# Optimization experiments

Measured on AMD Instinct MI355X. Metric: run time of the kernel, lower is better.

## Reference

```python
import jax, jax.numpy as jnp
import numpy as np
from jax import lax

N = 50000       # nodes
E = 1600000     # edges
D_IN = 1024     # input feature size
H = 256         # hidden size
L = 64          # GCN2Conv layers
C = 4           # n_classes
ALPHA = 0.2
THETA = 0.5


def setup_inputs() -> dict:
    key = jax.random.key(0)
    ks = jax.random.split(key, 7)
    x = jax.random.normal(ks[0], (N, D_IN), dtype=jnp.float32)
    edge_index = jax.random.randint(ks[1], (2, E), 0, N, dtype=jnp.int32)
    proj_W = jax.random.normal(ks[2], (D_IN, H), dtype=jnp.float32) * 0.02
    proj_b = jnp.zeros((H,), dtype=jnp.float32)
    weights = jax.random.normal(ks[3], (L, H, H), dtype=jnp.float32) * 0.05
    cls_W = jax.random.normal(ks[4], (H, C), dtype=jnp.float32) * 0.05
    cls_b = jnp.zeros((C,), dtype=jnp.float32)
    return {"x": x, "edge_index": edge_index, "proj_W": proj_W,
            "proj_b": proj_b, "weights": weights, "cls_W": cls_W, "cls_b": cls_b}


def reference(x, edge_index, proj_W, proj_b, weights, cls_W, cls_b):
    # Dropout is identity in eval mode (reference baseline).
    src, dst = edge_index[0], edge_index[1]
    # gcn_norm with added self-loops: A_hat = D^{-1/2} (A + I) D^{-1/2}
    loops = jnp.arange(N, dtype=src.dtype)
    src_f = jnp.concatenate([src, loops])
    dst_f = jnp.concatenate([dst, loops])
    deg = jax.ops.segment_sum(jnp.ones((E + N,), jnp.float32), dst_f, num_segments=N)
    dinv = jnp.where(deg > 0, lax.rsqrt(deg), 0.0)
    norm = dinv[src_f] * dinv[dst_f]  # [E+N]

    h0 = x @ proj_W + proj_b          # project: [N, H]
    betas = jnp.log(THETA / jnp.arange(1, L + 1, dtype=jnp.float32) + 1.0)  # [L]

    def step(h, wb):
        W, beta = wb
        # propagate: out[i] = sum_{(j->i)} norm * h[j]
        agg = jax.ops.segment_sum(norm[:, None] * h[src_f], dst_f, num_segments=N)
        s = (1.0 - ALPHA) * agg + ALPHA * h0     # initial residual
        h = (1.0 - beta) * s + beta * (s @ W)    # identity mapping (shared weights)
        return jax.nn.relu(h), None

    h, _ = lax.scan(step, h0, (weights, betas))
    out = h @ cls_W + cls_b  # classifier: [N, C]
    return out
```

## Files before the change

kernel.cpp:

```cpp
#include <hip/hip_runtime.h>
#include <math.h>

#define N_NODES 50000
#define N_EDGES 1600000
#define DIN 1024
#define H 256
#define L_LAYERS 64
#define ALPHA 0.2f
#define NCHUNK 8
#define CCOLS 32

typedef unsigned short u16;
typedef short short8 __attribute__((ext_vector_type(8)));
typedef unsigned short ushort8_t __attribute__((ext_vector_type(8)));
typedef float f32x4 __attribute__((ext_vector_type(4)));
typedef float f32x2 __attribute__((ext_vector_type(2)));
typedef unsigned int u32x4 __attribute__((ext_vector_type(4)));

__device__ inline float b2f(u16 h) { return __uint_as_float(((unsigned)h) << 16); }
__device__ inline u16 f2b(float f) {
  unsigned u = __float_as_uint(f);
  unsigned r = u + 0x7FFFu + ((u >> 16) & 1u);
  return (u16)(r >> 16);
}

__device__ inline f32x2 bp2f(unsigned u) {
  f32x2 p;
  p[0] = __uint_as_float(u << 16);
  p[1] = __uint_as_float(u & 0xFFFF0000u);
  return p;
}

__device__ inline size_t bidx(int node, int col) {
  return ((size_t)(col >> 5) * N_NODES + node) * CCOLS + (col & 31);
}

__global__ void GCNIIForDialog_18923625906417_kernel() {}

__global__ __launch_bounds__(256) void k_zero(int* __restrict__ p, int n) {
  int i = blockIdx.x * 256 + threadIdx.x;
  if (i < n) p[i] = 0;
}

__global__ __launch_bounds__(256) void k_count(const int* __restrict__ dst, int* __restrict__ cnt) {
  int e = blockIdx.x * 256 + threadIdx.x;
  if (e < N_EDGES) atomicAdd(&cnt[dst[e]], 1);
}

__global__ __launch_bounds__(256) void k_dinv(const int* __restrict__ cnt, float* __restrict__ dinv) {
  int i = blockIdx.x * 256 + threadIdx.x;
  if (i < N_NODES) dinv[i] = 1.0f / sqrtf((float)(cnt[i] + 1));
}

__global__ __launch_bounds__(1024) void k_scan(const int* __restrict__ cnt, int* __restrict__ offs) {
  const int CH = (N_NODES + 1023) / 1024;
  __shared__ int sums[1024];
  int t = threadIdx.x;
  int lo = t * CH, hi = lo + CH;
  if (hi > N_NODES) hi = N_NODES;
  int s = 0;
  for (int i = lo; i < hi; ++i) s += cnt[i];
  sums[t] = s;
  __syncthreads();
  for (int d = 1; d < 1024; d <<= 1) {
    int v = (t >= d) ? sums[t - d] : 0;
    __syncthreads();
    sums[t] += v;
    __syncthreads();
  }
  int run = (t == 0) ? 0 : sums[t - 1];
  for (int i = lo; i < hi; ++i) { offs[i] = run; run += cnt[i]; }
  if (t == 0) offs[N_NODES] = sums[1023];
}

__global__ __launch_bounds__(256) void k_scatter(const int* __restrict__ src, const int* __restrict__ dst,
    const int* __restrict__ offs, int* __restrict__ cursor, const float* __restrict__ dinv,
    unsigned* __restrict__ ew) {
  int e = blockIdx.x * 256 + threadIdx.x;
  if (e >= N_EDGES) return;
  int sN = src[e], dN = dst[e];
  int pos = offs[dN] + atomicAdd(&cursor[dN], 1);
  unsigned wb = (unsigned)f2b(dinv[sN] * dinv[dN]);
  ew[pos] = (wb << 16) | (unsigned)sN;
}

__global__ void k_wtr(const float* __restrict__ Win, u16* __restrict__ Wout) {
  __shared__ float tile[32][33];
  size_t base = (size_t)blockIdx.z * H * H;
  int n0 = blockIdx.x * 32, k0 = blockIdx.y * 32;
  for (int i = threadIdx.y; i < 32; i += 8)
    tile[i][threadIdx.x] = Win[base + (size_t)(k0 + i) * H + n0 + threadIdx.x];
  __syncthreads();
  for (int i = threadIdx.y; i < 32; i += 8)
    Wout[base + (size_t)(n0 + i) * H + k0 + threadIdx.x] = f2b(tile[threadIdx.x][i]);
}

__global__ void k_trP(const float* __restrict__ Win, u16* __restrict__ Wout) {
  __shared__ float tile[32][33];
  int n0 = blockIdx.x * 32, k0 = blockIdx.y * 32;
  for (int i = threadIdx.y; i < 32; i += 8)
    tile[i][threadIdx.x] = Win[(size_t)(k0 + i) * H + n0 + threadIdx.x];
  __syncthreads();
  for (int i = threadIdx.y; i < 32; i += 8)
    Wout[(size_t)(n0 + i) * DIN + k0 + threadIdx.x] = f2b(tile[threadIdx.x][i]);
}

__global__ __launch_bounds__(256) void k_spmm(
    const u16* __restrict__ hb, const u16* __restrict__ h0b,
    const int* __restrict__ offs, const unsigned* __restrict__ ew,
    const float* __restrict__ dinv, u16* __restrict__ sbb)
{
  int bid = blockIdx.x;
  int chunk = bid & 7;
  int nb = bid >> 3;
  int wid = threadIdx.x >> 6, lane = threadIdx.x & 63;
  int sub = lane & 3;
  int eslot = (lane >> 2) & 3;
  int nsub = lane >> 4;
  int node = nb * 16 + wid * 4 + nsub;
  if (node >= N_NODES) return;
  const u16* hc = hb + (size_t)chunk * N_NODES * CCOLS;
  const u16* hp = hc + sub * 8;
  f32x2 acc2[4] = {};
  int end = offs[node + 1];
  int i = offs[node] + eslot;
  for (; i + 12 < end; i += 16) {
    unsigned e0 = ew[i];
    unsigned e1 = ew[i + 4];
    unsigned e2 = ew[i + 8];
    unsigned e3 = ew[i + 12];
    u32x4 v0 = *(const u32x4*)(hp + (size_t)(e0 & 0xFFFFu) * CCOLS);
    u32x4 v1 = *(const u32x4*)(hp + (size_t)(e1 & 0xFFFFu) * CCOLS);
    u32x4 v2 = *(const u32x4*)(hp + (size_t)(e2 & 0xFFFFu) * CCOLS);
    u32x4 v3 = *(const u32x4*)(hp + (size_t)(e3 & 0xFFFFu) * CCOLS);
    float w0 = __uint_as_float(e0 & 0xFFFF0000u);
    float w1 = __uint_as_float(e1 & 0xFFFF0000u);
    float w2 = __uint_as_float(e2 & 0xFFFF0000u);
    float w3 = __uint_as_float(e3 & 0xFFFF0000u);
    f32x2 w0v = {w0, w0}, w1v = {w1, w1}, w2v = {w2, w2}, w3v = {w3, w3};
#pragma unroll
    for (int j = 0; j < 4; ++j) acc2[j] += w0v * bp2f(v0[j]);
#pragma unroll
    for (int j = 0; j < 4; ++j) acc2[j] += w1v * bp2f(v1[j]);
#pragma unroll
    for (int j = 0; j < 4; ++j) acc2[j] += w2v * bp2f(v2[j]);
#pragma unroll
    for (int j = 0; j < 4; ++j) acc2[j] += w3v * bp2f(v3[j]);
  }
  for (; i < end; i += 4) {
    unsigned e0 = ew[i];
    u32x4 v0 = *(const u32x4*)(hp + (size_t)(e0 & 0xFFFFu) * CCOLS);
    float w0 = __uint_as_float(e0 & 0xFFFF0000u);
    f32x2 w0v = {w0, w0};
#pragma unroll
    for (int j = 0; j < 4; ++j) acc2[j] += w0v * bp2f(v0[j]);
  }
#pragma unroll
  for (int d = 4; d <= 8; d <<= 1)
#pragma unroll
    for (int j = 0; j < 4; ++j) {
      acc2[j][0] += __shfl_xor(acc2[j][0], d);
      acc2[j][1] += __shfl_xor(acc2[j][1], d);
    }
  if (eslot == 0) {
    float di = dinv[node];
    float di2 = di * di;
    size_t ci = (size_t)chunk * N_NODES * CCOLS + (size_t)node * CCOLS + sub * 8;
    ushort8_t hv = *(const ushort8_t*)(hp + (size_t)node * CCOLS);
    ushort8_t h0v = __builtin_nontemporal_load((const ushort8_t*)(h0b + ci));
    ushort8_t o;
#pragma unroll
    for (int j = 0; j < 4; ++j) {
#pragma unroll
      for (int c = 0; c < 2; ++c) {
        int k = 2 * j + c;
        float v = (1.0f - ALPHA) * (acc2[j][c] + di2 * b2f(hv[k])) + ALPHA * b2f(h0v[k]);
        o[k] = f2b(v);
      }
    }
    __builtin_nontemporal_store(o, (ushort8_t*)(sbb + ci));
  }
}

__global__ __launch_bounds__(256) void k_gemm(
    const u16* __restrict__ A, const u16* __restrict__ BT,
    u16* __restrict__ Hout, float beta)
{
  __shared__ u16 As[128 * 40];
  __shared__ u16 Bs[128 * 40];
  int tid = threadIdx.x;
  int mBase = blockIdx.x * 128, nBase = blockIdx.y * 128;
  int wid = tid >> 6, lane = tid & 63;
  int wm = (wid & 1) * 64, wn = (wid >> 1) * 64;
  int lrow = lane & 15, quad = lane >> 4;
  f32x4 acc[4][4] = {};
  int sr = tid >> 2, sc = tid & 3;
  for (int k0 = 0; k0 < H; k0 += 32) {
    const u16* Ac = A + (size_t)(k0 >> 5) * N_NODES * CCOLS;
#pragma unroll
    for (int it = 0; it < 2; ++it) {
      int r = sr + it * 64;
      int grow = mBase + r;
      u32x4 va = {};
      if (grow < N_NODES) va = *(const u32x4*)(Ac + (size_t)grow * CCOLS + sc * 8);
      *(u32x4*)&As[r * 40 + sc * 8] = va;
      u32x4 vb = *(const u32x4*)(BT + (size_t)(nBase + r) * H + k0 + sc * 8);
      *(u32x4*)&Bs[r * 40 + sc * 8] = vb;
    }
    __syncthreads();
    short8 af[4], bfr[4];
#pragma unroll
    for (int i = 0; i < 4; ++i) {
      af[i]  = *(const short8*)&As[(wm + i * 16 + lrow) * 40 + quad * 8];
      bfr[i] = *(const short8*)&Bs[(wn + i * 16 + lrow) * 40 + quad * 8];
    }
#pragma unroll
    for (int mi = 0; mi < 4; ++mi)
#pragma unroll
      for (int ni = 0; ni < 4; ++ni)
        acc[mi][ni] = __builtin_amdgcn_mfma_f32_16x16x32_bf16(af[mi], bfr[ni], acc[mi][ni], 0, 0, 0);
    __syncthreads();
  }
#pragma unroll
  for (int mi = 0; mi < 4; ++mi)
#pragma unroll
    for (int ni = 0; ni < 4; ++ni)
#pragma unroll
      for (int rg = 0; rg < 4; ++rg) {
        int r = mBase + wm + mi * 16 + quad * 4 + rg;
        int c = nBase + wn + ni * 16 + lrow;
        if (r < N_NODES) {
          size_t idx = bidx(r, c);
          float v = (1.0f - beta) * b2f(A[idx]) + beta * acc[mi][ni][rg];
          Hout[idx] = f2b(fmaxf(v, 0.0f));
        }
      }
}

__global__ __launch_bounds__(256) void k_pgemm(
    const float* __restrict__ X, const u16* __restrict__ BT,
    const float* __restrict__ bias, u16* __restrict__ h0b, u16* __restrict__ h)
{
  __shared__ u16 As[128 * 40];
  __shared__ u16 Bs[128 * 40];
  int tid = threadIdx.x;
  int mBase = blockIdx.x * 128, nBase = blockIdx.y * 128;
  int wid = tid >> 6, lane = tid & 63;
  int wm = (wid & 1) * 64, wn = (wid >> 1) * 64;
  int lrow = lane & 15, quad = lane >> 4;
  f32x4 acc[4][4] = {};
  int sr = tid >> 2, sc = tid & 3;
  for (int k0 = 0; k0 < DIN; k0 += 32) {
#pragma unroll
    for (int it = 0; it < 2; ++it) {
      int r = sr + it * 64;
      int grow = mBase + r;
      float4 fa0 = make_float4(0.f, 0.f, 0.f, 0.f);
      float4 fa1 = make_float4(0.f, 0.f, 0.f, 0.f);
      if (grow < N_NODES) {
        const float* ap = X + (size_t)grow * DIN + k0 + sc * 8;
        fa0 = *(const float4*)ap;
        fa1 = *(const float4*)(ap + 4);
      }
      ushort8_t av;
      av[0] = f2b(fa0.x); av[1] = f2b(fa0.y); av[2] = f2b(fa0.z); av[3] = f2b(fa0.w);
      av[4] = f2b(fa1.x); av[5] = f2b(fa1.y); av[6] = f2b(fa1.z); av[7] = f2b(fa1.w);
      *(ushort8_t*)&As[r * 40 + sc * 8] = av;
      u32x4 vb = *(const u32x4*)(BT + (size_t)(nBase + r) * DIN + k0 + sc * 8);
      *(u32x4*)&Bs[r * 40 + sc * 8] = vb;
    }
    __syncthreads();
    short8 af[4], bfr[4];
#pragma unroll
    for (int i = 0; i < 4; ++i) {
      af[i]  = *(const short8*)&As[(wm + i * 16 + lrow) * 40 + quad * 8];
      bfr[i] = *(const short8*)&Bs[(wn + i * 16 + lrow) * 40 + quad * 8];
    }
#pragma unroll
    for (int mi = 0; mi < 4; ++mi)
#pragma unroll
      for (int ni = 0; ni < 4; ++ni)
        acc[mi][ni] = __builtin_amdgcn_mfma_f32_16x16x32_bf16(af[mi], bfr[ni], acc[mi][ni], 0, 0, 0);
    __syncthreads();
  }
#pragma unroll
  for (int mi = 0; mi < 4; ++mi)
#pragma unroll
    for (int ni = 0; ni < 4; ++ni)
#pragma unroll
      for (int rg = 0; rg < 4; ++rg) {
        int r = mBase + wm + mi * 16 + quad * 4 + rg;
        int c = nBase + wn + ni * 16 + lrow;
        if (r < N_NODES) {
          size_t idx = bidx(r, c);
          float v = acc[mi][ni][rg] + bias[c];
          u16 bv = f2b(v);
          h0b[idx] = bv;
          h[idx] = bv;
        }
      }
}

__global__ __launch_bounds__(256) void k_cls(const u16* __restrict__ h,
    const float* __restrict__ W, const float* __restrict__ b, float* __restrict__ out)
{
  int wid = threadIdx.x >> 6, lane = threadIdx.x & 63;
  int node = blockIdx.x * 4 + wid;
  if (node >= N_NODES) return;
  float a0 = 0, a1 = 0, a2 = 0, a3 = 0;
  for (int t = lane; t < H; t += 64) {
    float hv = b2f(h[bidx(node, t)]);
    a0 += hv * W[t * 4 + 0];
    a1 += hv * W[t * 4 + 1];
    a2 += hv * W[t * 4 + 2];
    a3 += hv * W[t * 4 + 3];
  }
#pragma unroll
  for (int off = 32; off > 0; off >>= 1) {
    a0 += __shfl_down(a0, off);
    a1 += __shfl_down(a1, off);
    a2 += __shfl_down(a2, off);
    a3 += __shfl_down(a3, off);
  }
  if (lane == 0) {
    float4 o;
    o.x = a0 + b[0];
    o.y = a1 + b[1];
    o.z = a2 + b[2];
    o.w = a3 + b[3];
    *(float4*)(out + (size_t)node * 4) = o;
  }
}

extern "C" void kernel_launch(void* const* d_in, const int* in_sizes, int n_in,
                              void* d_out, int out_size, void* d_ws, size_t ws_size,
                              hipStream_t stream) {
  (void)in_sizes; (void)n_in; (void)out_size; (void)ws_size;
  const float* x     = (const float*)d_in[0];
  const int*   ei    = (const int*)d_in[1];
  const float* projW = (const float*)d_in[2];
  const float* projB = (const float*)d_in[3];
  const float* wts   = (const float*)d_in[4];
  const float* clsW  = (const float*)d_in[5];
  const float* clsB  = (const float*)d_in[6];
  float* out = (float*)d_out;

  char* ws = (char*)d_ws;
  size_t off = 0;
  auto alloc = [&](size_t bytes) -> void* {
    void* p = ws + off;
    off = (off + bytes + 255) & ~(size_t)255;
    return p;
  };
  int*   cntcur = (int*)alloc((size_t)N_NODES * 2 * 4);
  int*   cnt    = cntcur;
  int*   cursor = cntcur + N_NODES;
  int*   offs   = (int*)alloc((size_t)(N_NODES + 1) * 4);
  float* dinv   = (float*)alloc((size_t)N_NODES * 4);
  unsigned* ew  = (unsigned*)alloc((size_t)N_EDGES * 4);
  u16*   WT     = (u16*)alloc((size_t)L_LAYERS * H * H * 2);
  u16*   BTp    = (u16*)alloc((size_t)H * DIN * 2);
  u16*   h0b    = (u16*)alloc((size_t)N_NODES * H * 2);
  u16*   sb     = (u16*)alloc((size_t)N_NODES * H * 2);
  u16*   h      = (u16*)alloc((size_t)N_NODES * H * 2);

  const int* src = ei;
  const int* dst = ei + N_EDGES;

  k_zero<<<(N_NODES * 2 + 255) / 256, 256, 0, stream>>>(cntcur, N_NODES * 2);
  k_count<<<(N_EDGES + 255) / 256, 256, 0, stream>>>(dst, cnt);
  k_dinv<<<(N_NODES + 255) / 256, 256, 0, stream>>>(cnt, dinv);
  k_scan<<<1, 1024, 0, stream>>>(cnt, offs);
  k_scatter<<<(N_EDGES + 255) / 256, 256, 0, stream>>>(src, dst, offs, cursor, dinv, ew);
  k_wtr<<<dim3(H / 32, H / 32, L_LAYERS), dim3(32, 8), 0, stream>>>(wts, WT);
  k_trP<<<dim3(H / 32, DIN / 32), dim3(32, 8), 0, stream>>>(projW, BTp);

  k_pgemm<<<dim3((N_NODES + 127) / 128, H / 128), 256, 0, stream>>>(x, BTp, projB, h0b, h);

  dim3 ggrid((N_NODES + 127) / 128, H / 128);
  const int spmm_blocks = ((N_NODES + 15) / 16) * NCHUNK;
  for (int l = 0; l < L_LAYERS; ++l) {
    k_spmm<<<spmm_blocks, 256, 0, stream>>>(h, h0b, offs, ew, dinv, sb);
    float beta = logf(0.5f / (float)(l + 1) + 1.0f);
    k_gemm<<<ggrid, 256, 0, stream>>>(sb, WT + (size_t)l * H * H, h, beta);
  }
  k_cls<<<(N_NODES + 3) / 4, 256, 0, stream>>>(h, clsW, clsB, out);
}
```

Measured before the change: 9.419 ms.

## Pad CSR rows to multiples of four and use persistent SpMM blocks

Each node's edge list in the CSR is padded to a multiple of four, with the edge array zero-filled so padding entries carry weight zero and point at node 0. Each lane can then fetch four packed edges with one 128-bit nontemporal load and the scalar tail loop goes away. The SpMM kernel also becomes a grid-stride kernel with a fixed 2048 blocks that loop over node groups per chunk, which cuts block launch overhead. The cost is extra zero-weight gathers on node 0 and a larger edge array that needs an extra zeroing pass.

Result: slower. 11.52 ms (+22.3%).

```diff
diff --git a/kernel.cpp b/kernel.cpp
--- a/kernel.cpp
+++ b/kernel.cpp
@@ -9,6 +9,9 @@
 #define ALPHA 0.2f
 #define NCHUNK 8
 #define CCOLS 32
+#define EW_CAP (N_EDGES + 4 * N_NODES)
+#define SPMM_BLOCKS 2048
+#define BLK_PER_CHUNK (SPMM_BLOCKS / NCHUNK)
 
 typedef unsigned short u16;
 typedef short short8 __attribute__((ext_vector_type(8)));
@@ -59,7 +62,7 @@
   int lo = t * CH, hi = lo + CH;
   if (hi > N_NODES) hi = N_NODES;
   int s = 0;
-  for (int i = lo; i < hi; ++i) s += cnt[i];
+  for (int i = lo; i < hi; ++i) s += (cnt[i] + 3) & ~3;
   sums[t] = s;
   __syncthreads();
   for (int d = 1; d < 1024; d <<= 1) {
@@ -69,7 +72,7 @@
     __syncthreads();
   }
   int run = (t == 0) ? 0 : sums[t - 1];
-  for (int i = lo; i < hi; ++i) { offs[i] = run; run += cnt[i]; }
+  for (int i = lo; i < hi; ++i) { offs[i] = run; run += (cnt[i] + 3) & ~3; }
   if (t == 0) offs[N_NODES] = sums[1023];
 }
 
@@ -110,75 +113,66 @@
     const int* __restrict__ offs, const unsigned* __restrict__ ew,
     const float* __restrict__ dinv, u16* __restrict__ sbb)
 {
-  int bid = blockIdx.x;
-  int chunk = bid & 7;
-  int nb = bid >> 3;
+  const int NBLK = (N_NODES + 15) / 16;
+  int chunk = blockIdx.x & 7;
+  int bslot = blockIdx.x >> 3;
   int wid = threadIdx.x >> 6, lane = threadIdx.x & 63;
   int sub = lane & 3;
   int eslot = (lane >> 2) & 3;
   int nsub = lane >> 4;
-  int node = nb * 16 + wid * 4 + nsub;
-  if (node >= N_NODES) return;
   const u16* hc = hb + (size_t)chunk * N_NODES * CCOLS;
   const u16* hp = hc + sub * 8;
-  f32x2 acc2[4] = {};
-  int end = offs[node + 1];
-  int i = offs[node] + eslot;
-  for (; i + 12 < end; i += 16) {
-    unsigned e0 = ew[i];
-    unsigned e1 = ew[i + 4];
-    unsigned e2 = ew[i + 8];
-    unsigned e3 = ew[i + 12];
-    u32x4 v0 = *(const u32x4*)(hp + (size_t)(e0 & 0xFFFFu) * CCOLS);
-    u32x4 v1 = *(const u32x4*)(hp + (size_t)(e1 & 0xFFFFu) * CCOLS);
-    u32x4 v2 = *(const u32x4*)(hp + (size_t)(e2 & 0xFFFFu) * CCOLS);
-    u32x4 v3 = *(const u32x4*)(hp + (size_t)(e3 & 0xFFFFu) * CCOLS);
-    float w0 = __uint_as_float(e0 & 0xFFFF0000u);
-    float w1 = __uint_as_float(e1 & 0xFFFF0000u);
-    float w2 = __uint_as_float(e2 & 0xFFFF0000u);
-    float w3 = __uint_as_float(e3 & 0xFFFF0000u);
-    f32x2 w0v = {w0, w0}, w1v = {w1, w1}, w2v = {w2, w2}, w3v = {w3, w3};
-#pragma unroll
-    for (int j = 0; j < 4; ++j) acc2[j] += w0v * bp2f(v0[j]);
-#pragma unroll
-    for (int j = 0; j < 4; ++j) acc2[j] += w1v * bp2f(v1[j]);
-#pragma unroll
-    for (int j = 0; j < 4; ++j) acc2[j] += w2v * bp2f(v2[j]);
-#pragma unroll
-    for (int j = 0; j < 4; ++j) acc2[j] += w3v * bp2f(v3[j]);
-  }
-  for (; i < end; i += 4) {
-    unsigned e0 = ew[i];
-    u32x4 v0 = *(const u32x4*)(hp + (size_t)(e0 & 0xFFFFu) * CCOLS);
-    float w0 = __uint_as_float(e0 & 0xFFFF0000u);
-    f32x2 w0v = {w0, w0};
-#pragma unroll
-    for (int j = 0; j < 4; ++j) acc2[j] += w0v * bp2f(v0[j]);
-  }
-#pragma unroll
-  for (int d = 4; d <= 8; d <<= 1)
-#pragma unroll
-    for (int j = 0; j < 4; ++j) {
-      acc2[j][0] += __shfl_xor(acc2[j][0], d);
-      acc2[j][1] += __shfl_xor(acc2[j][1], d);
-    }
-  if (eslot == 0) {
-    float di = dinv[node];
-    float di2 = di * di;
-    size_t ci = (size_t)chunk * N_NODES * CCOLS + (size_t)node * CCOLS + sub * 8;
-    ushort8_t hv = *(const ushort8_t*)(hp + (size_t)node * CCOLS);
-    ushort8_t h0v = __builtin_nontemporal_load((const ushort8_t*)(h0b + ci));
-    ushort8_t o;
-#pragma unroll
-    for (int j = 0; j < 4; ++j) {
-#pragma unroll
-      for (int c = 0; c < 2; ++c) {
-        int k = 2 * j + c;
-        float v = (1.0f - ALPHA) * (acc2[j][c] + di2 * b2f(hv[k])) + ALPHA * b2f(h0v[k]);
-        o[k] = f2b(v);
-      }
-    }
-    __builtin_nontemporal_store(o, (ushort8_t*)(sbb + ci));
+
+  for (int nb = bslot; nb < NBLK; nb += BLK_PER_CHUNK) {
+    int node = nb * 16 + wid * 4 + nsub;
+    if (node >= N_NODES) continue;
+    f32x2 acc2[4] = {};
+    int i0 = offs[node], end = offs[node + 1];
+    for (int i = i0 + eslot * 4; i < end; i += 16) {
+      u32x4 er = __builtin_nontemporal_load((const u32x4*)(ew + i));
+      u32x4 v0 = *(const u32x4*)(hp + (size_t)(er[0] & 0xFFFFu) * CCOLS);
+      u32x4 v1 = *(const u32x4*)(hp + (size_t)(er[1] & 0xFFFFu) * CCOLS);
+      u32x4 v2 = *(const u32x4*)(hp + (size_t)(er[2] & 0xFFFFu) * CCOLS);
+      u32x4 v3 = *(const u32x4*)(hp + (size_t)(er[3] & 0xFFFFu) * CCOLS);
+      float w0 = __uint_as_float(er[0] & 0xFFFF0000u);
+      float w1 = __uint_as_float(er[1] & 0xFFFF0000u);
+      float w2 = __uint_as_float(er[2] & 0xFFFF0000u);
+      float w3 = __uint_as_float(er[3] & 0xFFFF0000u);
+      f32x2 w0v = {w0, w0}, w1v = {w1, w1}, w2v = {w2, w2}, w3v = {w3, w3};
+#pragma unroll
+      for (int j = 0; j < 4; ++j) acc2[j] += w0v * bp2f(v0[j]);
+#pragma unroll
+      for (int j = 0; j < 4; ++j) acc2[j] += w1v * bp2f(v1[j]);
+#pragma unroll
+      for (int j = 0; j < 4; ++j) acc2[j] += w2v * bp2f(v2[j]);
+#pragma unroll
+      for (int j = 0; j < 4; ++j) acc2[j] += w3v * bp2f(v3[j]);
+    }
+#pragma unroll
+    for (int d = 4; d <= 8; d <<= 1)
+#pragma unroll
+      for (int j = 0; j < 4; ++j) {
+        acc2[j][0] += __shfl_xor(acc2[j][0], d);
+        acc2[j][1] += __shfl_xor(acc2[j][1], d);
+      }
+    if (eslot == 0) {
+      float di = dinv[node];
+      float di2 = di * di;
+      size_t ci = (size_t)chunk * N_NODES * CCOLS + (size_t)node * CCOLS + sub * 8;
+      ushort8_t hv = *(const ushort8_t*)(hp + (size_t)node * CCOLS);
+      ushort8_t h0v = __builtin_nontemporal_load((const ushort8_t*)(h0b + ci));
+      ushort8_t o;
+#pragma unroll
+      for (int j = 0; j < 4; ++j) {
+#pragma unroll
+        for (int c = 0; c < 2; ++c) {
+          int k = 2 * j + c;
+          float v = (1.0f - ALPHA) * (acc2[j][c] + di2 * b2f(hv[k])) + ALPHA * b2f(h0v[k]);
+          o[k] = f2b(v);
+        }
+      }
+      __builtin_nontemporal_store(o, (ushort8_t*)(sbb + ci));
+    }
   }
 }
 
@@ -357,7 +351,7 @@
   int*   cursor = cntcur + N_NODES;
   int*   offs   = (int*)alloc((size_t)(N_NODES + 1) * 4);
   float* dinv   = (float*)alloc((size_t)N_NODES * 4);
-  unsigned* ew  = (unsigned*)alloc((size_t)N_EDGES * 4);
+  unsigned* ew  = (unsigned*)alloc((size_t)EW_CAP * 4);
   u16*   WT     = (u16*)alloc((size_t)L_LAYERS * H * H * 2);
   u16*   BTp    = (u16*)alloc((size_t)H * DIN * 2);
   u16*   h0b    = (u16*)alloc((size_t)N_NODES * H * 2);
@@ -368,6 +362,7 @@
   const int* dst = ei + N_EDGES;
 
   k_zero<<<(N_NODES * 2 + 255) / 256, 256, 0, stream>>>(cntcur, N_NODES * 2);
+  k_zero<<<(EW_CAP + 255) / 256, 256, 0, stream>>>((int*)ew, EW_CAP);
   k_count<<<(N_EDGES + 255) / 256, 256, 0, stream>>>(dst, cnt);
   k_dinv<<<(N_NODES + 255) / 256, 256, 0, stream>>>(cnt, dinv);
   k_scan<<<1, 1024, 0, stream>>>(cnt, offs);
@@ -378,9 +373,8 @@
   k_pgemm<<<dim3((N_NODES + 127) / 128, H / 128), 256, 0, stream>>>(x, BTp, projB, h0b, h);
 
   dim3 ggrid((N_NODES + 127) / 128, H / 128);
-  const int spmm_blocks = ((N_NODES + 15) / 16) * NCHUNK;
   for (int l = 0; l < L_LAYERS; ++l) {
-    k_spmm<<<spmm_blocks, 256, 0, stream>>>(h, h0b, offs, ew, dinv, sb);
+    k_spmm<<<SPMM_BLOCKS, 256, 0, stream>>>(h, h0b, offs, ew, dinv, sb);
     float beta = logf(0.5f / (float)(l + 1) + 1.0f);
     k_gemm<<<ggrid, 256, 0, stream>>>(sb, WT + (size_t)l * H * H, h, beta);
   }
```

## Fuse SpMM aggregation and layer GEMM into one kernel with LDS-resident tile

Applied to the files above, without the earlier changes.

Merges the per-layer sparse aggregation and dense GEMM into a single kernel: each block aggregates 128 nodes across all 256 columns into shared memory, then multiplies that tile by the full weight matrix in two column halves. This removes the intermediate s buffer round trip through global memory and one launch per layer, and uses ping-pong h buffers because the gather reads h from other nodes. In exchange, grid parallelism drops from ~25k small SpMM blocks to ~391 large blocks with ~68KB of LDS each, limiting occupancy and latency hiding for the irregular gathers.

After: 19.98 ms. 2.12x slower.

```diff
diff --git a/kernel.cpp b/kernel.cpp
--- a/kernel.cpp
+++ b/kernel.cpp
@@ -9,6 +9,7 @@
 #define ALPHA 0.2f
 #define NCHUNK 8
 #define CCOLS 32
+#define SBS_STRIDE 268
 
 typedef unsigned short u16;
 typedef short short8 __attribute__((ext_vector_type(8)));
@@ -105,136 +106,140 @@
     Wout[(size_t)(n0 + i) * DIN + k0 + threadIdx.x] = f2b(tile[threadIdx.x][i]);
 }
 
-__global__ __launch_bounds__(256) void k_spmm(
+__global__ __launch_bounds__(256) void k_fused(
     const u16* __restrict__ hb, const u16* __restrict__ h0b,
     const int* __restrict__ offs, const unsigned* __restrict__ ew,
-    const float* __restrict__ dinv, u16* __restrict__ sbb)
-{
-  int bid = blockIdx.x;
-  int chunk = bid & 7;
-  int nb = bid >> 3;
-  int wid = threadIdx.x >> 6, lane = threadIdx.x & 63;
-  int sub = lane & 3;
-  int eslot = (lane >> 2) & 3;
-  int nsub = lane >> 4;
-  int node = nb * 16 + wid * 4 + nsub;
-  if (node >= N_NODES) return;
-  const u16* hc = hb + (size_t)chunk * N_NODES * CCOLS;
-  const u16* hp = hc + sub * 8;
-  f32x2 acc2[4] = {};
-  int end = offs[node + 1];
-  int i = offs[node] + eslot;
-  for (; i + 12 < end; i += 16) {
-    unsigned e0 = ew[i];
-    unsigned e1 = ew[i + 4];
-    unsigned e2 = ew[i + 8];
-    unsigned e3 = ew[i + 12];
-    u32x4 v0 = *(const u32x4*)(hp + (size_t)(e0 & 0xFFFFu) * CCOLS);
-    u32x4 v1 = *(const u32x4*)(hp + (size_t)(e1 & 0xFFFFu) * CCOLS);
-    u32x4 v2 = *(const u32x4*)(hp + (size_t)(e2 & 0xFFFFu) * CCOLS);
-    u32x4 v3 = *(const u32x4*)(hp + (size_t)(e3 & 0xFFFFu) * CCOLS);
-    float w0 = __uint_as_float(e0 & 0xFFFF0000u);
-    float w1 = __uint_as_float(e1 & 0xFFFF0000u);
-    float w2 = __uint_as_float(e2 & 0xFFFF0000u);
-    float w3 = __uint_as_float(e3 & 0xFFFF0000u);
-    f32x2 w0v = {w0, w0}, w1v = {w1, w1}, w2v = {w2, w2}, w3v = {w3, w3};
-#pragma unroll
-    for (int j = 0; j < 4; ++j) acc2[j] += w0v * bp2f(v0[j]);
-#pragma unroll
-    for (int j = 0; j < 4; ++j) acc2[j] += w1v * bp2f(v1[j]);
-#pragma unroll
-    for (int j = 0; j < 4; ++j) acc2[j] += w2v * bp2f(v2[j]);
-#pragma unroll
-    for (int j = 0; j < 4; ++j) acc2[j] += w3v * bp2f(v3[j]);
-  }
-  for (; i < end; i += 4) {
-    unsigned e0 = ew[i];
-    u32x4 v0 = *(const u32x4*)(hp + (size_t)(e0 & 0xFFFFu) * CCOLS);
-    float w0 = __uint_as_float(e0 & 0xFFFF0000u);
-    f32x2 w0v = {w0, w0};
-#pragma unroll
-    for (int j = 0; j < 4; ++j) acc2[j] += w0v * bp2f(v0[j]);
-  }
-#pragma unroll
-  for (int d = 4; d <= 8; d <<= 1)
-#pragma unroll
-    for (int j = 0; j < 4; ++j) {
-      acc2[j][0] += __shfl_xor(acc2[j][0], d);
-      acc2[j][1] += __shfl_xor(acc2[j][1], d);
-    }
-  if (eslot == 0) {
-    float di = dinv[node];
-    float di2 = di * di;
-    size_t ci = (size_t)chunk * N_NODES * CCOLS + (size_t)node * CCOLS + sub * 8;
-    ushort8_t hv = *(const ushort8_t*)(hp + (size_t)node * CCOLS);
-    ushort8_t h0v = __builtin_nontemporal_load((const ushort8_t*)(h0b + ci));
-    ushort8_t o;
-#pragma unroll
-    for (int j = 0; j < 4; ++j) {
-#pragma unroll
-      for (int c = 0; c < 2; ++c) {
-        int k = 2 * j + c;
-        float v = (1.0f - ALPHA) * (acc2[j][c] + di2 * b2f(hv[k])) + ALPHA * b2f(h0v[k]);
-        o[k] = f2b(v);
-      }
-    }
-    __builtin_nontemporal_store(o, (ushort8_t*)(sbb + ci));
-  }
-}
-
-__global__ __launch_bounds__(256) void k_gemm(
-    const u16* __restrict__ A, const u16* __restrict__ BT,
+    const float* __restrict__ dinv, const u16* __restrict__ BT,
     u16* __restrict__ Hout, float beta)
 {
-  __shared__ u16 As[128 * 40];
+  __shared__ u16 sbs[128][SBS_STRIDE];
   __shared__ u16 Bs[128 * 40];
   int tid = threadIdx.x;
-  int mBase = blockIdx.x * 128, nBase = blockIdx.y * 128;
   int wid = tid >> 6, lane = tid & 63;
+  int mBase = blockIdx.x * 128;
+
+  {
+    int sub = lane & 3;
+    int eslot = (lane >> 2) & 3;
+    int nsub = lane >> 4;
+    for (int chunk = 0; chunk < NCHUNK; ++chunk) {
+      const u16* hc = hb + (size_t)chunk * N_NODES * CCOLS;
+      const u16* hp = hc + sub * 8;
+      for (int pass = 0; pass < 8; ++pass) {
+        int lr = wid * 32 + pass * 4 + nsub;
+        int node = mBase + lr;
+        bool valid = node < N_NODES;
+        f32x2 acc2[4] = {};
+        if (valid) {
+          int end = offs[node + 1];
+          int i = offs[node] + eslot;
+          for (; i + 12 < end; i += 16) {
+            unsigned e0 = ew[i];
+            unsigned e1 = ew[i + 4];
+            unsigned e2 = ew[i + 8];
+            unsigned e3 = ew[i + 12];
+            u32x4 v0 = *(const u32x4*)(hp + (size_t)(e0 & 0xFFFFu) * CCOLS);
+            u32x4 v1 = *(const u32x4*)(hp + (size_t)(e1 & 0xFFFFu) * CCOLS);
+            u32x4 v2 = *(const u32x4*)(hp + (size_t)(e2 & 0xFFFFu) * CCOLS);
+            u32x4 v3 = *(const u32x4*)(hp + (size_t)(e3 & 0xFFFFu) * CCOLS);
+            float w0 = __uint_as_float(e0 & 0xFFFF0000u);
+            float w1 = __uint_as_float(e1 & 0xFFFF0000u);
+            float w2 = __uint_as_float(e2 & 0xFFFF0000u);
+            float w3 = __uint_as_float(e3 & 0xFFFF0000u);
+            f32x2 w0v = {w0, w0}, w1v = {w1, w1}, w2v = {w2, w2}, w3v = {w3, w3};
+#pragma unroll
+            for (int j = 0; j < 4; ++j) acc2[j] += w0v * bp2f(v0[j]);
+#pragma unroll
+            for (int j = 0; j < 4; ++j) acc2[j] += w1v * bp2f(v1[j]);
+#pragma unroll
+            for (int j = 0; j < 4; ++j) acc2[j] += w2v * bp2f(v2[j]);
+#pragma unroll
+            for (int j = 0; j < 4; ++j) acc2[j] += w3v * bp2f(v3[j]);
+          }
+          for (; i < end; i += 4) {
+            unsigned e0 = ew[i];
+            u32x4 v0 = *(const u32x4*)(hp + (size_t)(e0 & 0xFFFFu) * CCOLS);
+            float w0 = __uint_as_float(e0 & 0xFFFF0000u);
+            f32x2 w0v = {w0, w0};
+#pragma unroll
+            for (int j = 0; j < 4; ++j) acc2[j] += w0v * bp2f(v0[j]);
+          }
+        }
+#pragma unroll
+        for (int d = 4; d <= 8; d <<= 1)
+#pragma unroll
+          for (int j = 0; j < 4; ++j) {
+            acc2[j][0] += __shfl_xor(acc2[j][0], d);
+            acc2[j][1] += __shfl_xor(acc2[j][1], d);
+          }
+        if (eslot == 0) {
+          ushort8_t o = {0, 0, 0, 0, 0, 0, 0, 0};
+          if (valid) {
+            float di = dinv[node];
+            float di2 = di * di;
+            size_t ci = (size_t)chunk * N_NODES * CCOLS + (size_t)node * CCOLS + sub * 8;
+            ushort8_t hv = *(const ushort8_t*)(hp + (size_t)node * CCOLS);
+            ushort8_t h0v = __builtin_nontemporal_load((const ushort8_t*)(h0b + ci));
+#pragma unroll
+            for (int j = 0; j < 4; ++j) {
+#pragma unroll
+              for (int c = 0; c < 2; ++c) {
+                int k = 2 * j + c;
+                float v = (1.0f - ALPHA) * (acc2[j][c] + di2 * b2f(hv[k])) + ALPHA * b2f(h0v[k]);
+                o[k] = f2b(v);
+              }
+            }
+          }
+          *(ushort8_t*)&sbs[lr][chunk * 32 + sub * 8] = o;
+        }
+      }
+    }
+  }
+  __syncthreads();
+
   int wm = (wid & 1) * 64, wn = (wid >> 1) * 64;
   int lrow = lane & 15, quad = lane >> 4;
-  f32x4 acc[4][4] = {};
   int sr = tid >> 2, sc = tid & 3;
-  for (int k0 = 0; k0 < H; k0 += 32) {
-    const u16* Ac = A + (size_t)(k0 >> 5) * N_NODES * CCOLS;
-#pragma unroll
-    for (int it = 0; it < 2; ++it) {
-      int r = sr + it * 64;
-      int grow = mBase + r;
-      u32x4 va = {};
-      if (grow < N_NODES) va = *(const u32x4*)(Ac + (size_t)grow * CCOLS + sc * 8);
-      *(u32x4*)&As[r * 40 + sc * 8] = va;
-      u32x4 vb = *(const u32x4*)(BT + (size_t)(nBase + r) * H + k0 + sc * 8);
-      *(u32x4*)&Bs[r * 40 + sc * 8] = vb;
+  for (int nh = 0; nh < 2; ++nh) {
+    int nBase = nh * 128;
+    f32x4 acc[4][4] = {};
+    for (int k0 = 0; k0 < H; k0 += 32) {
+#pragma unroll
+      for (int it = 0; it < 2; ++it) {
+        int r = sr + it * 64;
+        u32x4 vb = *(const u32x4*)(BT + (size_t)(nBase + r) * H + k0 + sc * 8);
+        *(u32x4*)&Bs[r * 40 + sc * 8] = vb;
+      }
+      __syncthreads();
+      short8 af[4], bfr[4];
+#pragma unroll
+      for (int i = 0; i < 4; ++i) {
+        af[i]  = *(const short8*)&sbs[wm + i * 16 + lrow][k0 + quad * 8];
+        bfr[i] = *(const short8*)&Bs[(wn + i * 16 + lrow) * 40 + quad * 8];
+      }
+#pragma unroll
+      for (int mi = 0; mi < 4; ++mi)
+#pragma unroll
+        for (int ni = 0; ni < 4; ++ni)
+          acc[mi][ni] = __builtin_amdgcn_mfma_f32_16x16x32_bf16(af[mi], bfr[ni], acc[mi][ni], 0, 0, 0);
+      __syncthreads();
     }
-    __syncthreads();
-    short8 af[4], bfr[4];
-#pragma unroll
-    for (int i = 0; i < 4; ++i) {
-      af[i]  = *(const short8*)&As[(wm + i * 16 + lrow) * 40 + quad * 8];
-      bfr[i] = *(const short8*)&Bs[(wn + i * 16 + lrow) * 40 + quad * 8];
-    }
 #pragma unroll
     for (int mi = 0; mi < 4; ++mi)
 #pragma unroll
       for (int ni = 0; ni < 4; ++ni)
-        acc[mi][ni] = __builtin_amdgcn_mfma_f32_16x16x32_bf16(af[mi], bfr[ni], acc[mi][ni], 0, 0, 0);
-    __syncthreads();
-  }
-#pragma unroll
-  for (int mi = 0; mi < 4; ++mi)
-#pragma unroll
-    for (int ni = 0; ni < 4; ++ni)
-#pragma unroll
-      for (int rg = 0; rg < 4; ++rg) {
-        int r = mBase + wm + mi * 16 + quad * 4 + rg;
-        int c = nBase + wn + ni * 16 + lrow;
-        if (r < N_NODES) {
-          size_t idx = bidx(r, c);
-          float v = (1.0f - beta) * b2f(A[idx]) + beta * acc[mi][ni][rg];
-          Hout[idx] = f2b(fmaxf(v, 0.0f));
+#pragma unroll
+        for (int rg = 0; rg < 4; ++rg) {
+          int lr = wm + mi * 16 + quad * 4 + rg;
+          int r = mBase + lr;
+          int c = nBase + wn + ni * 16 + lrow;
+          if (r < N_NODES) {
+            float s = b2f(sbs[lr][c]);
+            float v = (1.0f - beta) * s + beta * acc[mi][ni][rg];
+            Hout[bidx(r, c)] = f2b(fmaxf(v, 0.0f));
+          }
         }
-      }
+  }
 }
 
 __global__ __launch_bounds__(256) void k_pgemm(
@@ -361,8 +366,8 @@
   u16*   WT     = (u16*)alloc((size_t)L_LAYERS * H * H * 2);
   u16*   BTp    = (u16*)alloc((size_t)H * DIN * 2);
   u16*   h0b    = (u16*)alloc((size_t)N_NODES * H * 2);
-  u16*   sb     = (u16*)alloc((size_t)N_NODES * H * 2);
-  u16*   h      = (u16*)alloc((size_t)N_NODES * H * 2);
+  u16*   hA     = (u16*)alloc((size_t)N_NODES * H * 2);
+  u16*   hB     = (u16*)alloc((size_t)N_NODES * H * 2);
 
   const int* src = ei;
   const int* dst = ei + N_EDGES;
@@ -375,14 +380,15 @@
   k_wtr<<<dim3(H / 32, H / 32, L_LAYERS), dim3(32, 8), 0, stream>>>(wts, WT);
   k_trP<<<dim3(H / 32, DIN / 32), dim3(32, 8), 0, stream>>>(projW, BTp);
 
-  k_pgemm<<<dim3((N_NODES + 127) / 128, H / 128), 256, 0, stream>>>(x, BTp, projB, h0b, h);
-
-  dim3 ggrid((N_NODES + 127) / 128, H / 128);
-  const int spmm_blocks = ((N_NODES + 15) / 16) * NCHUNK;
+  k_pgemm<<<dim3((N_NODES + 127) / 128, H / 128), 256, 0, stream>>>(x, BTp, projB, h0b, hA);
+
+  const int fgrid = (N_NODES + 127) / 128;
   for (int l = 0; l < L_LAYERS; ++l) {
-    k_spmm<<<spmm_blocks, 256, 0, stream>>>(h, h0b, offs, ew, dinv, sb);
+    const u16* hin = (l & 1) ? hB : hA;
+    u16* hout      = (l & 1) ? hA : hB;
     float beta = logf(0.5f / (float)(l + 1) + 1.0f);
-    k_gemm<<<ggrid, 256, 0, stream>>>(sb, WT + (size_t)l * H * H, h, beta);
-  }
-  k_cls<<<(N_NODES + 3) / 4, 256, 0, stream>>>(h, clsW, clsB, out);
-}
+    k_fused<<<fgrid, 256, 0, stream>>>(hin, h0b, offs, ew, dinv,
+                                       WT + (size_t)l * H * H, hout, beta);
+  }
+  k_cls<<<(N_NODES + 3) / 4, 256, 0, stream>>>(hA, clsW, clsB, out);
+}
```
